# Kernel tuning notes

Hardware: AMD Instinct MI355X
Metric: run time of the kernel (lower is better)

## Reference

```python
import jax, jax.numpy as jnp
import numpy as np

SYM_LIST = jnp.array([0, 7, 12, 20], dtype=jnp.int32)
B, N = 128, 1000


def setup_inputs() -> dict:
    key = jax.random.key(0)
    k1, k2, k3, k4, k5 = jax.random.split(key, 5)
    return {
        "pred_r": jax.random.normal(k1, (B, 3, 3), dtype=jnp.float32),
        "pred_t": jax.random.normal(k2, (B, 1, 3), dtype=jnp.float32),
        "targets": jax.random.normal(k3, (B, N, 3), dtype=jnp.float32),
        "model_points": jax.random.normal(k4, (B, N, 3), dtype=jnp.float32),
        "idxs": jax.random.randint(k5, (B,), 0, 21, dtype=jnp.int32),
    }


def reference(pred_r, pred_t, targets, model_points, idxs):
    # rigid transform: model_points @ pred_r^T + pred_t  -> [B, N, 3]
    pred_points = jnp.einsum("bni,bji->bnj", model_points, pred_r) + pred_t

    # batched nearest-neighbor search (cdist + argmin), vectorized over batch
    # squared distances [B, N, N]: d2[b,i,j] = ||pred[b,i] - tgt[b,j]||^2
    p2 = jnp.sum(pred_points * pred_points, axis=-1, keepdims=True)      # [B,N,1]
    t2 = jnp.sum(targets * targets, axis=-1, keepdims=True)             # [B,N,1]
    d2 = p2 + jnp.swapaxes(t2, 1, 2) - 2.0 * jnp.einsum(
        "bnd,bmd->bnm", pred_points, targets)
    inds = jnp.argmin(d2, axis=-1)                                       # [B,N]

    # gather nearest targets; apply only for symmetric object ids
    tgt_knn = jnp.take_along_axis(targets, inds[..., None], axis=1)      # [B,N,3]
    is_sym = jnp.isin(idxs, SYM_LIST)                                    # [B]
    tgt = jnp.where(is_sym[:, None, None], tgt_knn, targets)

    # mean over points of L2 norm, then mean over batch -> scalar
    dis = jnp.mean(jnp.linalg.norm(pred_points - tgt, axis=2), axis=1).mean()
    return dis
```

## Files before the change

kernel.cpp:

```cpp
#include <hip/hip_runtime.h>
#include <float.h>


#define BATCH 128
#define NPTS  1000
#define SPLIT 16
#define PTS_PER_BLK 64
#define LANES_PER_PT 4
#define JCHUNK (NPTS / LANES_PER_PT)
#define THREADS 256

__global__ __launch_bounds__(THREADS) void pose_loss_kernel(
    const float* __restrict__ pred_r,
    const float* __restrict__ pred_t,
    const float* __restrict__ targets,
    const float* __restrict__ model_points,
    const int*   __restrict__ idxs,
    float* __restrict__ out)
{
    const int b   = blockIdx.x / SPLIT;
    const int s   = blockIdx.x % SPLIT;
    const int tid = threadIdx.x;

    const int id = idxs[b];
    const bool sym = (id == 0) | (id == 7) | (id == 12) | (id == 20);

    const float* Rb = pred_r + b * 9;
    const float* Tb = pred_t + b * 3;
    const float R00 = Rb[0], R01 = Rb[1], R02 = Rb[2];
    const float R10 = Rb[3], R11 = Rb[4], R12 = Rb[5];
    const float R20 = Rb[6], R21 = Rb[7], R22 = Rb[8];
    const float T0 = Tb[0], T1 = Tb[1], T2 = Tb[2];

    __shared__ float4 tsh[NPTS];
    if (sym) {
        const float* tb = targets + (size_t)b * 3 * NPTS;
        for (int k = tid; k < NPTS; k += THREADS) {
            const float x = tb[3 * k + 0];
            const float y = tb[3 * k + 1];
            const float z = tb[3 * k + 2];
            tsh[k] = make_float4(x, y, z, fmaf(x, x, fmaf(y, y, z * z)));
        }
        __syncthreads();
    }

    const int iloc = tid >> 2;
    const int sub  = tid & 3;
    const int i    = s * PTS_PER_BLK + iloc;

    float acc = 0.0f;
    if (i < NPTS) {
        const float* mp = model_points + ((size_t)b * NPTS + i) * 3;
        const float m0 = mp[0], m1 = mp[1], m2 = mp[2];
        const float px = fmaf(m0, R00, fmaf(m1, R01, fmaf(m2, R02, T0)));
        const float py = fmaf(m0, R10, fmaf(m1, R11, fmaf(m2, R12, T1)));
        const float pz = fmaf(m0, R20, fmaf(m1, R21, fmaf(m2, R22, T2)));

        if (sym) {
            float bestd = FLT_MAX;
            int   bestj = sub * JCHUNK;
            const int j0 = sub * JCHUNK;
            #pragma unroll 5
            for (int j = j0; j < j0 + JCHUNK; ++j) {
                const float4 q = tsh[j];
                const float dot = fmaf(px, q.x, fmaf(py, q.y, pz * q.z));
                const float d2  = fmaf(-2.0f, dot, q.w);
                if (d2 < bestd) { bestd = d2; bestj = j; }
            }
            #pragma unroll
            for (int off = 1; off < LANES_PER_PT; off <<= 1) {
                const float od = __shfl_xor(bestd, off, 64);
                const int   oj = __shfl_xor(bestj, off, 64);
                if (od < bestd || (od == bestd && oj < bestj)) {
                    bestd = od; bestj = oj;
                }
            }
            if (sub == 0) {
                const float4 q = tsh[bestj];
                const float dx = px - q.x, dy = py - q.y, dz = pz - q.z;
                acc = sqrtf(fmaf(dx, dx, fmaf(dy, dy, dz * dz)));
            }
        } else if (sub == 0) {
            const float* tg = targets + ((size_t)b * NPTS + i) * 3;
            const float dx = px - tg[0], dy = py - tg[1], dz = pz - tg[2];
            acc = sqrtf(fmaf(dx, dx, fmaf(dy, dy, dz * dz)));
        }
    }

    #pragma unroll
    for (int off = 32; off > 0; off >>= 1)
        acc += __shfl_down(acc, off, 64);

    __shared__ float wsum[THREADS / 64];
    const int wid = tid >> 6, lane = tid & 63;
    if (lane == 0) wsum[wid] = acc;
    __syncthreads();
    if (tid == 0) {
        float s2 = 0.0f;
        #pragma unroll
        for (int w = 0; w < THREADS / 64; ++w) s2 += wsum[w];
        atomicAdd(out, s2 * (1.0f / (BATCH * NPTS)));
    }
}

extern "C" void kernel_launch(void* const* d_in, const int* in_sizes, int n_in,
                              void* d_out, int out_size, void* d_ws, size_t ws_size,
                              hipStream_t stream) {
    const float* pred_r       = (const float*)d_in[0];
    const float* pred_t       = (const float*)d_in[1];
    const float* targets      = (const float*)d_in[2];
    const float* model_points = (const float*)d_in[3];
    const int*   idxs         = (const int*)d_in[4];
    float* out = (float*)d_out;

    hipMemsetAsync(out, 0, sizeof(float) * out_size, stream);

    pose_loss_kernel<<<BATCH * SPLIT, THREADS, 0, stream>>>(
        pred_r, pred_t, targets, model_points, idxs, out);
}
```

Baseline: 96.33 us.

## Use 8 lanes per point with 512 threads and two-pass reduction instead of atomics

Doubles the number of lanes cooperating on each point's nearest-neighbor scan, so each lane scans 125 targets instead of 250, and doubles the block size to 512 threads. Replaces the memset and the per-block float atomicAdd with per-block partial sums written to the workspace, followed by a single-block reduction kernel. This shortens the serial argmin loop per thread and removes atomic contention, at the cost of an extra kernel launch and one more shuffle step per point.

```diff
diff --git a/kernel.cpp b/kernel.cpp
--- a/kernel.cpp
+++ b/kernel.cpp
@@ -6,9 +6,10 @@
 #define NPTS  1000
 #define SPLIT 16
 #define PTS_PER_BLK 64
-#define LANES_PER_PT 4
+#define LANES_PER_PT 8
 #define JCHUNK (NPTS / LANES_PER_PT)
-#define THREADS 256
+#define THREADS 512
+#define NBLK (BATCH * SPLIT)
 
 __global__ __launch_bounds__(THREADS) void pose_loss_kernel(
     const float* __restrict__ pred_r,
@@ -16,7 +17,7 @@
     const float* __restrict__ targets,
     const float* __restrict__ model_points,
     const int*   __restrict__ idxs,
-    float* __restrict__ out)
+    float* __restrict__ partial)
 {
     const int b   = blockIdx.x / SPLIT;
     const int s   = blockIdx.x % SPLIT;
@@ -35,6 +36,7 @@
     __shared__ float4 tsh[NPTS];
     if (sym) {
         const float* tb = targets + (size_t)b * 3 * NPTS;
+        #pragma unroll
         for (int k = tid; k < NPTS; k += THREADS) {
             const float x = tb[3 * k + 0];
             const float y = tb[3 * k + 1];
@@ -44,8 +46,8 @@
         __syncthreads();
     }
 
-    const int iloc = tid >> 2;
-    const int sub  = tid & 3;
+    const int iloc = tid >> 3;
+    const int sub  = tid & 7;
     const int i    = s * PTS_PER_BLK + iloc;
 
     float acc = 0.0f;
@@ -99,7 +101,30 @@
         float s2 = 0.0f;
         #pragma unroll
         for (int w = 0; w < THREADS / 64; ++w) s2 += wsum[w];
-        atomicAdd(out, s2 * (1.0f / (BATCH * NPTS)));
+        partial[blockIdx.x] = s2;
+    }
+}
+
+__global__ __launch_bounds__(256) void pose_loss_reduce(
+    const float* __restrict__ partial,
+    float* __restrict__ out)
+{
+    const int tid = threadIdx.x;
+    float acc = 0.0f;
+    #pragma unroll
+    for (int k = tid; k < NBLK; k += 256) acc += partial[k];
+
+    #pragma unroll
+    for (int off = 32; off > 0; off >>= 1)
+        acc += __shfl_down(acc, off, 64);
+
+    __shared__ float wsum[4];
+    const int wid = tid >> 6, lane = tid & 63;
+    if (lane == 0) wsum[wid] = acc;
+    __syncthreads();
+    if (tid == 0) {
+        float s2 = wsum[0] + wsum[1] + wsum[2] + wsum[3];
+        out[0] = s2 * (1.0f / (BATCH * NPTS));
     }
 }
 
@@ -111,10 +136,10 @@
     const float* targets      = (const float*)d_in[2];
     const float* model_points = (const float*)d_in[3];
     const int*   idxs         = (const int*)d_in[4];
-    float* out = (float*)d_out;
+    float* out     = (float*)d_out;
+    float* partial = (float*)d_ws;
 
-    hipMemsetAsync(out, 0, sizeof(float) * out_size, stream);
-
-    pose_loss_kernel<<<BATCH * SPLIT, THREADS, 0, stream>>>(
-        pred_r, pred_t, targets, model_points, idxs, out);
+    pose_loss_kernel<<<NBLK, THREADS, 0, stream>>>(
+        pred_r, pred_t, targets, model_points, idxs, partial);
+    pose_loss_reduce<<<1, 256, 0, stream>>>(partial, out);
 }
```

Measured after the change: 77.82 us. 1.24x faster.
